# Optimization experiments

Hardware: AMD Instinct MI355X
Metric: run time of the kernel (lower is better)

The kernel has to match this reference:

```python
import jax, jax.numpy as jnp
import numpy as np
from jax import lax

GAMMA_MIN = 1e-4
BIG = 1e9  # finite stand-in for +inf so softmin grads stay nan-free


def _cosine_cost(a, b):
    # F.normalize(dim=-1) with eps=1e-12, then 1 - a_n @ b_n.T
    an = a / jnp.maximum(jnp.linalg.norm(a, axis=-1, keepdims=True), 1e-12)
    bn = b / jnp.maximum(jnp.linalg.norm(b, axis=-1, keepdims=True), 1e-12)
    return 1.0 - an @ bn.T  # (M, N)


def _shift1(v):
    # v[i-1] with BIG padding at i=0
    return jnp.concatenate([jnp.full((1,), BIG, v.dtype), v[:-1]])


def _softdtw(cost, g):
    # Anti-diagonal wavefront DP. Diagonal d holds R[i, d-i], stored as a
    # length-(M+1) vector indexed by i. R[0,0]=0, borders = BIG (inf).
    M, N = cost.shape
    i_arr = jnp.arange(M + 1)
    r0 = jnp.full(M + 1, BIG, cost.dtype).at[0].set(0.0)  # diagonal d=0
    r1 = jnp.full(M + 1, BIG, cost.dtype)                 # diagonal d=1

    def step(carry, d):
        r_dm2, r_dm1 = carry  # diagonals d-2 and d-1
        j = d - i_arr
        valid = (i_arr >= 1) & (i_arr <= M) & (j >= 1) & (j <= N)
        c = cost[jnp.clip(i_arr - 1, 0, M - 1), jnp.clip(j - 1, 0, N - 1)]
        diag = _shift1(r_dm2)   # R[i-1, j-1]
        above = _shift1(r_dm1)  # R[i-1, j]
        left = r_dm1            # R[i,   j-1]
        v = jnp.stack([diag, above, left])  # (3, M+1)
        smin = -g * jax.nn.logsumexp(-v / g, axis=0)
        r_new = jnp.where(valid, c + smin, BIG)
        return (r_dm1, r_new), None

    ds = jnp.arange(2, M + N + 1)
    (_, r_last), _ = lax.scan(step, (r0, r1), ds)
    return r_last[M]  # R[M, N]


def setup_inputs() -> dict:
    key = jax.random.key(0)
    kx, ky = jax.random.split(key)
    M, N, D = 2048, 2048, 1024
    x = jax.random.normal(kx, (M, D), dtype=jnp.float32)
    y = jax.random.normal(ky, (N, D), dtype=jnp.float32)
    gamma = jnp.array(1.0, dtype=jnp.float32)  # learned nn.Parameter
    return {"x": x, "y": y, "gamma": gamma}


def reference(x, y, gamma):
    g = jnp.maximum(jnp.abs(gamma), GAMMA_MIN)
    sdtw = _softdtw(_cosine_cost(x, y), g)
    # normalize=True: subtract 0.5*(sdtw(x,x) + sdtw(y,y))
    sdtw_xx = _softdtw(_cosine_cost(x, x), g)
    sdtw_yy = _softdtw(_cosine_cost(y, y), g)
    return sdtw - 0.5 * (sdtw_xx + sdtw_yy)
```

## Files before the change

### kernel.cpp

```cpp
#include <hip/hip_runtime.h>
#include <hip/hip_bf16.h>
#include <math.h>

#define MDIM 2048
#define KDIM 1024
#define BIGF 1e9f
#define NSTRIP 32

typedef unsigned short ushort;
typedef unsigned int uint;
typedef __attribute__((ext_vector_type(8))) short short8v;
typedef __attribute__((ext_vector_type(8))) ushort ushort8v;
typedef __attribute__((ext_vector_type(4))) float f32x4;
typedef __attribute__((ext_vector_type(4), aligned(4))) float f4u;

__device__ __forceinline__ ushort f2bf(float f) {
  uint b = __builtin_bit_cast(uint, f);
  b += 0x7FFFu + ((b >> 16) & 1u);
  return (ushort)(b >> 16);
}

__global__ __launch_bounds__(256) void normalize_rows(
    const float* __restrict__ x, const float* __restrict__ y,
    ushort* __restrict__ xb, ushort* __restrict__ yb) {
  int wave = (blockIdx.x * blockDim.x + threadIdx.x) >> 6;
  int lane = threadIdx.x & 63;
  const float* src;
  ushort* dst;
  int row;
  if (wave < MDIM) { src = x; dst = xb; row = wave; }
  else             { src = y; dst = yb; row = wave - MDIM; }
  const float* r = src + (size_t)row * KDIM;
  ushort* w = dst + (size_t)row * KDIM;
  float ss = 0.f;
  for (int c = lane * 4; c < KDIM; c += 64 * 4) {
    float4 v = *(const float4*)&r[c];
    ss += v.x * v.x + v.y * v.y + v.z * v.z + v.w * v.w;
  }
  #pragma unroll
  for (int off = 32; off; off >>= 1) ss += __shfl_xor(ss, off, 64);
  float inv = 1.f / fmaxf(sqrtf(ss), 1e-12f);
  for (int c = lane * 4; c < KDIM; c += 64 * 4) {
    float4 v = *(const float4*)&r[c];
    uint2 o;
    o.x = (uint)f2bf(v.x * inv) | ((uint)f2bf(v.y * inv) << 16);
    o.y = (uint)f2bf(v.z * inv) | ((uint)f2bf(v.w * inv) << 16);
    *(uint2*)&w[c] = o;
  }
}

__global__ __launch_bounds__(256) void gemm_cost_mfma(
    const ushort* __restrict__ xb, const ushort* __restrict__ yb,
    float* __restrict__ cost_base, const float* __restrict__ gamma_p) {
  int z = blockIdx.z;
  const ushort* A = (z == 2) ? yb : xb;
  const ushort* B = (z == 0) ? yb : ((z == 1) ? xb : yb);
  float* C = cost_base + (size_t)z * MDIM * MDIM;
  float g = fmaxf(fabsf(gamma_p[0]), 1e-4f);
  float kexp = 1.44269504089f / g;

  __shared__ ushort As[128 * 64];
  __shared__ ushort Bs[128 * 64];

  int tid = threadIdx.x;
  int w = tid >> 6, l = tid & 63;
  int wr = w >> 1, wc = w & 1;
  int abase = blockIdx.y * 128;
  int bbase = blockIdx.x * 128;

  f32x4 acc[4][4] = {};

  for (int k0 = 0; k0 < KDIM; k0 += 64) {
    ushort8v va[4], vb[4];
    #pragma unroll
    for (int q = 0; q < 4; ++q) {
      int slot = q * 256 + tid;
      int row = slot >> 3, sc = slot & 7;
      va[q] = *(const ushort8v*)&A[(size_t)(abase + row) * KDIM + k0 + sc * 8];
      vb[q] = *(const ushort8v*)&B[(size_t)(bbase + row) * KDIM + k0 + sc * 8];
    }
    __syncthreads();
    #pragma unroll
    for (int q = 0; q < 4; ++q) {
      int slot = q * 256 + tid;
      int row = slot >> 3, sc = slot & 7;
      int off = row * 64 + ((sc ^ (row & 7)) << 3);
      *(ushort8v*)&As[off] = va[q];
      *(ushort8v*)&Bs[off] = vb[q];
    }
    __syncthreads();
    #pragma unroll
    for (int kk = 0; kk < 2; ++kk) {
      short8v af[4], bf[4];
      #pragma unroll
      for (int m = 0; m < 4; ++m) {
        int row = wr * 64 + m * 16 + (l & 15);
        int kg = kk * 4 + (l >> 4);
        af[m] = *(const short8v*)&As[row * 64 + ((kg ^ (row & 7)) << 3)];
      }
      #pragma unroll
      for (int n = 0; n < 4; ++n) {
        int row = wc * 64 + n * 16 + (l & 15);
        int kg = kk * 4 + (l >> 4);
        bf[n] = *(const short8v*)&Bs[row * 64 + ((kg ^ (row & 7)) << 3)];
      }
      #pragma unroll
      for (int m = 0; m < 4; ++m)
        #pragma unroll
        for (int n = 0; n < 4; ++n)
          acc[m][n] = __builtin_amdgcn_mfma_f32_16x16x32_bf16(
              af[m], bf[n], acc[m][n], 0, 0, 0);
    }
  }
  #pragma unroll
  for (int m = 0; m < 4; ++m) {
    int row0 = abase + wr * 64 + m * 16 + (l >> 4) * 4;
    #pragma unroll
    for (int n = 0; n < 4; ++n) {
      int col = bbase + wc * 64 + n * 16 + (l & 15);
      f32x4 v = acc[m][n];
      #pragma unroll
      for (int r = 0; r < 4; ++r)
        C[(size_t)(row0 + r) * MDIM + col] = (1.0f - v[r]) * kexp;
    }
  }
}

__device__ __forceinline__ float fexp2(float x) { return __builtin_amdgcn_exp2f(x); }
__device__ __forceinline__ float flog2(float x) { return __builtin_amdgcn_logf(x); }

__device__ __forceinline__ float shr1(float v) {
  int r = __builtin_amdgcn_update_dpp(__builtin_bit_cast(int, v),
                                      __builtin_bit_cast(int, v),
                                      0x138 , 0xF, 0xF, false);
  return __builtin_bit_cast(float, r);
}

__device__ __forceinline__ float aload(const float* p) {
  return __hip_atomic_load(p, __ATOMIC_RELAXED, __HIP_MEMORY_SCOPE_AGENT);
}

__device__ __forceinline__ void stage(f4u (&buf)[16],
                                      const float* __restrict__ crow, int base) {
  #pragma unroll
  for (int k = 0; k < 16; ++k)
    buf[k] = *(const f4u*)&crow[base + 4 * k];
}

__device__ __forceinline__ void stage_edge(f4u (&buf)[16],
                                           const float* __restrict__ crow,
                                           int base) {
  #pragma unroll
  for (int k = 0; k < 16; ++k)
    #pragma unroll
    for (int j = 0; j < 4; ++j) {
      int col = min(max(base + 4 * k + j, 0), MDIM - 1);
      buf[k][j] = crow[col];
    }
}

template <bool FIRST, bool EDGE>
__device__ __forceinline__ void phase_body(
    float& o, float& d, float bqv, const f4u (&cur)[16],
    int cb, int lane, float* __restrict__ bw) {
  const bool l0 = (lane == 0);
  const bool l63 = (lane == 63);
  float h0, h1, h2, h3;
  #pragma unroll
  for (int u = 0; u < 64; ++u) {
    float t = shr1(o);
    float av;
    if (FIRST) {
      av = l0 ? BIGF : t;
    } else {
      float rv = __builtin_bit_cast(
          float, __builtin_amdgcn_readlane(__builtin_bit_cast(int, bqv), u));
      av = l0 ? rv : t;
    }
    float mn, md, mx;
    asm("v_min3_f32 %0, %1, %2, %3" : "=v"(mn) : "v"(d), "v"(av), "v"(o));
    asm("v_med3_f32 %0, %1, %2, %3" : "=v"(md) : "v"(d), "v"(av), "v"(o));
    asm("v_max3_f32 %0, %1, %2, %3" : "=v"(mx) : "v"(d), "v"(av), "v"(o));
    float e = 1.0f + fexp2(mn - md) + fexp2(mn - mx);
    float n = cur[u >> 2][u & 3] + (mn - flog2(e));
    if (EDGE) {
      int c = cb + u - lane;
      bool valid = ((unsigned)c < (unsigned)MDIM);
      n = valid ? n : BIGF;
      if (l63 && valid) bw[c] = n;
    } else {
      if ((u & 3) == 0) h0 = n;
      else if ((u & 3) == 1) h1 = n;
      else if ((u & 3) == 2) h2 = n;
      else {
        h3 = n;
        if (l63) *(f4u*)&bw[cb + u - 66] = (f4u){h0, h1, h2, h3};
      }
    }
    d = av;
    o = n;
  }
}

__global__ __launch_bounds__(64, 1) void softdtw_dp(
    const float* __restrict__ cost_base, float* __restrict__ bottom,
    int* __restrict__ flags) {
  const int bid = blockIdx.x;
  const int z = bid & 7;
  if (z >= 3) return;
  const int s = bid >> 3;
  const int lane = threadIdx.x;

  const float* cost = cost_base + (size_t)z * MDIM * MDIM;
  const float* crow = cost + (size_t)(s * 64 + lane) * MDIM;
  float* bot_z = bottom + (size_t)z * NSTRIP * MDIM;
  const float* bp = bot_z + (size_t)(s > 0 ? s - 1 : 0) * MDIM;
  float* bw = bot_z + (size_t)s * MDIM;
  int* predf = &flags[z * NSTRIP + (s > 0 ? s - 1 : 0)];
  int* myf = &flags[z * NSTRIP + s];

  const int pS0 = 2 * s;
  const int pS1 = 2 * s + 32;

  f4u bufA[16], bufB[16];
  stage_edge(bufA, crow, -lane);

  float o = BIGF;
  float d = (s == 0 && lane == 0) ? 0.0f : BIGF;

  if (lane == 63 && s > 0)
    __hip_atomic_store(myf, pS0, __ATOMIC_RELEASE, __HIP_MEMORY_SCOPE_AGENT);

  int pcache = 0;
  for (int p = pS0; p <= pS1; ++p) {
    const int dq = p - pS0;
    const int cb = dq << 6;
    if (s > 0 && pcache < p) {
      int it = 0;
      do {
        pcache = __hip_atomic_load(predf, __ATOMIC_ACQUIRE,
                                   __HIP_MEMORY_SCOPE_AGENT);
        if (pcache < p) __builtin_amdgcn_s_sleep(1);
      } while (pcache < p && ++it < (1 << 22));
    }
    float bqv = 0.0f;
    if (s > 0) bqv = aload(&bp[min(cb + lane, MDIM - 1)]);
    if (dq < 31) {
      if ((dq & 1) == 0) stage(bufB, crow, cb + 64 - lane);
      else               stage(bufA, crow, cb + 64 - lane);
    } else if (dq == 31) {
      stage_edge(bufA, crow, cb + 64 - lane);
    }
    const bool edge = (dq == 0) || (dq == 32);
    if (s == 0) {
      if ((dq & 1) == 0) {
        if (edge) phase_body<true, true>(o, d, bqv, bufA, cb, lane, bw);
        else      phase_body<true, false>(o, d, bqv, bufA, cb, lane, bw);
      } else {
        phase_body<true, false>(o, d, bqv, bufB, cb, lane, bw);
      }
    } else {
      if ((dq & 1) == 0) {
        if (edge) phase_body<false, true>(o, d, bqv, bufA, cb, lane, bw);
        else      phase_body<false, false>(o, d, bqv, bufA, cb, lane, bw);
      } else {
        phase_body<false, false>(o, d, bqv, bufB, cb, lane, bw);
      }
    }
    if (lane == 63)
      __hip_atomic_store(myf, p + 1, __ATOMIC_RELEASE,
                         __HIP_MEMORY_SCOPE_AGENT);
  }
  if (lane == 63)
    __hip_atomic_store(myf, 1 << 20, __ATOMIC_RELEASE,
                       __HIP_MEMORY_SCOPE_AGENT);
}

__global__ void dtw_init(int* __restrict__ flags) {
  if (threadIdx.x < 3 * NSTRIP) flags[threadIdx.x] = 0;
}

__global__ void combine(const float* __restrict__ bottom,
                        const float* __restrict__ gamma_p,
                        float* __restrict__ out) {
  float g = fmaxf(fabsf(gamma_p[0]), 1e-4f);
  float glog = 0.69314718056f * g;
  float b0 = bottom[0 * NSTRIP * MDIM + (NSTRIP - 1) * MDIM + 2047];
  float b1 = bottom[1 * NSTRIP * MDIM + (NSTRIP - 1) * MDIM + 2047];
  float b2 = bottom[2 * NSTRIP * MDIM + (NSTRIP - 1) * MDIM + 2047];
  out[0] = (b0 - 0.5f * (b1 + b2)) * glog;
}

extern "C" void kernel_launch(void* const* d_in, const int* in_sizes, int n_in,
                              void* d_out, int out_size, void* d_ws, size_t ws_size,
                              hipStream_t stream) {
  const float* x = (const float*)d_in[0];
  const float* y = (const float*)d_in[1];
  const float* gamma = (const float*)d_in[2];
  float* out = (float*)d_out;

  char* ws = (char*)d_ws;
  ushort* xb = (ushort*)ws;
  ushort* yb = (ushort*)(ws + (size_t)4 * 1024 * 1024);
  float* cost = (float*)(ws + (size_t)8 * 1024 * 1024);
  float* bottom = (float*)(ws + (size_t)56 * 1024 * 1024);
  int* flags = (int*)(ws + (size_t)59 * 1024 * 1024);

  normalize_rows<<<(2 * MDIM) / 4, 256, 0, stream>>>(x, y, xb, yb);

  dim3 ggrid(MDIM / 128, MDIM / 128, 3);
  gemm_cost_mfma<<<ggrid, 256, 0, stream>>>(xb, yb, cost, gamma);

  dtw_init<<<1, 128, 0, stream>>>(flags);

  softdtw_dp<<<256, 64, 0, stream>>>(cost, bottom, flags);

  combine<<<1, 1, 0, stream>>>(bottom, gamma, out);
}
```

Baseline: 887.0 us.

## Halve DP phase granularity to 32 columns to shorten inter-strip pipeline latency

Each strip now advances in phases of 32 anti-diagonal steps instead of 64, with 66 phases per strip, and signals the next strip after each one. Successor strips can start sooner, which shortens the fill and drain of the 32-strip wavefront pipeline. The next cost tile and the boundary value are prefetched one phase ahead, with a sched_barrier and a register pin to keep the loads overlapped with compute. The cost is twice as many flag polls and atomic stores, and smaller prefetch batches.

```diff
diff --git a/kernel.cpp b/kernel.cpp
--- a/kernel.cpp
+++ b/kernel.cpp
@@ -140,18 +140,24 @@
   return __hip_atomic_load(p, __ATOMIC_RELAXED, __HIP_MEMORY_SCOPE_AGENT);
 }
 
-__device__ __forceinline__ void stage(f4u (&buf)[16],
-                                      const float* __restrict__ crow, int base) {
-  #pragma unroll
-  for (int k = 0; k < 16; ++k)
+__device__ __forceinline__ void pin8(f4u (&b)[8]) {
+  asm volatile("" : "+v"(b[0]), "+v"(b[1]), "+v"(b[2]), "+v"(b[3]),
+                    "+v"(b[4]), "+v"(b[5]), "+v"(b[6]), "+v"(b[7]));
+}
+
+__device__ __forceinline__ void stage8(f4u (&buf)[8],
+                                       const float* __restrict__ crow,
+                                       int base) {
+  #pragma unroll
+  for (int k = 0; k < 8; ++k)
     buf[k] = *(const f4u*)&crow[base + 4 * k];
 }
 
-__device__ __forceinline__ void stage_edge(f4u (&buf)[16],
-                                           const float* __restrict__ crow,
-                                           int base) {
-  #pragma unroll
-  for (int k = 0; k < 16; ++k)
+__device__ __forceinline__ void stage8_edge(f4u (&buf)[8],
+                                            const float* __restrict__ crow,
+                                            int base) {
+  #pragma unroll
+  for (int k = 0; k < 8; ++k)
     #pragma unroll
     for (int j = 0; j < 4; ++j) {
       int col = min(max(base + 4 * k + j, 0), MDIM - 1);
@@ -160,21 +166,21 @@
 }
 
 template <bool FIRST, bool EDGE>
-__device__ __forceinline__ void phase_body(
-    float& o, float& d, float bqv, const f4u (&cur)[16],
+__device__ __forceinline__ void phase32(
+    float& o, float& d, float bq, const f4u (&cur)[8],
     int cb, int lane, float* __restrict__ bw) {
   const bool l0 = (lane == 0);
   const bool l63 = (lane == 63);
   float h0, h1, h2, h3;
   #pragma unroll
-  for (int u = 0; u < 64; ++u) {
+  for (int u = 0; u < 32; ++u) {
     float t = shr1(o);
     float av;
     if (FIRST) {
       av = l0 ? BIGF : t;
     } else {
       float rv = __builtin_bit_cast(
-          float, __builtin_amdgcn_readlane(__builtin_bit_cast(int, bqv), u));
+          float, __builtin_amdgcn_readlane(__builtin_bit_cast(int, bq), u));
       av = l0 ? rv : t;
     }
     float mn, md, mx;
@@ -202,6 +208,61 @@
   }
 }
 
+template <bool FIRST>
+__device__ __forceinline__ void do_phase(
+    int dq, int s, int lane, f4u (&cur)[8], f4u (&nxt)[8],
+    float& o, float& d, float& bqN,
+    const float* __restrict__ crow, const float* __restrict__ bp,
+    float* __restrict__ bw, int* myf, int* predf, int& pcache) {
+  const int p = 4 * s + dq;
+  const int cb = dq << 5;
+  if (!FIRST && pcache < p) {
+    int it = 0;
+    do {
+      pcache = __hip_atomic_load(predf, __ATOMIC_ACQUIRE,
+                                 __HIP_MEMORY_SCOPE_AGENT);
+      if (pcache < p) __builtin_amdgcn_s_sleep(1);
+    } while (pcache < p && ++it < (1 << 22));
+  }
+  float bq = bqN;
+  if (dq >= 1 && dq <= 62)      stage8(nxt, crow, cb + 32 - lane);
+  else if (dq != 65)            stage8_edge(nxt, crow, cb + 32 - lane);
+  if (!FIRST && dq < 65)
+    bqN = aload(&bp[min(cb + 32 + lane, MDIM - 1)]);
+  __builtin_amdgcn_sched_barrier(0);
+  pin8(cur);
+  const bool edge = (dq < 2) || (dq > 63);
+  if (edge) phase32<FIRST, true>(o, d, bq, cur, cb, lane, bw);
+  else      phase32<FIRST, false>(o, d, bq, cur, cb, lane, bw);
+  if (lane == 63)
+    __hip_atomic_store(myf, p + 1, __ATOMIC_RELEASE,
+                       __HIP_MEMORY_SCOPE_AGENT);
+}
+
+template <bool FIRST>
+__device__ __forceinline__ void run_strip(
+    int s, int lane, const float* __restrict__ crow,
+    const float* __restrict__ bp, float* __restrict__ bw,
+    int* myf, int* predf) {
+  f4u bufA[8], bufB[8];
+  stage8_edge(bufA, crow, -lane);
+  float o = BIGF;
+  float d = (FIRST && lane == 0) ? 0.0f : BIGF;
+  float bqN = 0.0f;
+  if (!FIRST) bqN = aload(&bp[lane]);
+  int pcache = 0;
+  #pragma unroll 1
+  for (int dq2 = 0; dq2 < 66; dq2 += 2) {
+    do_phase<FIRST>(dq2, s, lane, bufA, bufB, o, d, bqN, crow, bp, bw,
+                    myf, predf, pcache);
+    do_phase<FIRST>(dq2 + 1, s, lane, bufB, bufA, o, d, bqN, crow, bp, bw,
+                    myf, predf, pcache);
+  }
+  if (lane == 63)
+    __hip_atomic_store(myf, 1 << 20, __ATOMIC_RELEASE,
+                       __HIP_MEMORY_SCOPE_AGENT);
+}
+
 __global__ __launch_bounds__(64, 1) void softdtw_dp(
     const float* __restrict__ cost_base, float* __restrict__ bottom,
     int* __restrict__ flags) {
@@ -219,61 +280,8 @@
   int* predf = &flags[z * NSTRIP + (s > 0 ? s - 1 : 0)];
   int* myf = &flags[z * NSTRIP + s];
 
-  const int pS0 = 2 * s;
-  const int pS1 = 2 * s + 32;
-
-  f4u bufA[16], bufB[16];
-  stage_edge(bufA, crow, -lane);
-
-  float o = BIGF;
-  float d = (s == 0 && lane == 0) ? 0.0f : BIGF;
-
-  if (lane == 63 && s > 0)
-    __hip_atomic_store(myf, pS0, __ATOMIC_RELEASE, __HIP_MEMORY_SCOPE_AGENT);
-
-  int pcache = 0;
-  for (int p = pS0; p <= pS1; ++p) {
-    const int dq = p - pS0;
-    const int cb = dq << 6;
-    if (s > 0 && pcache < p) {
-      int it = 0;
-      do {
-        pcache = __hip_atomic_load(predf, __ATOMIC_ACQUIRE,
-                                   __HIP_MEMORY_SCOPE_AGENT);
-        if (pcache < p) __builtin_amdgcn_s_sleep(1);
-      } while (pcache < p && ++it < (1 << 22));
-    }
-    float bqv = 0.0f;
-    if (s > 0) bqv = aload(&bp[min(cb + lane, MDIM - 1)]);
-    if (dq < 31) {
-      if ((dq & 1) == 0) stage(bufB, crow, cb + 64 - lane);
-      else               stage(bufA, crow, cb + 64 - lane);
-    } else if (dq == 31) {
-      stage_edge(bufA, crow, cb + 64 - lane);
-    }
-    const bool edge = (dq == 0) || (dq == 32);
-    if (s == 0) {
-      if ((dq & 1) == 0) {
-        if (edge) phase_body<true, true>(o, d, bqv, bufA, cb, lane, bw);
-        else      phase_body<true, false>(o, d, bqv, bufA, cb, lane, bw);
-      } else {
-        phase_body<true, false>(o, d, bqv, bufB, cb, lane, bw);
-      }
-    } else {
-      if ((dq & 1) == 0) {
-        if (edge) phase_body<false, true>(o, d, bqv, bufA, cb, lane, bw);
-        else      phase_body<false, false>(o, d, bqv, bufA, cb, lane, bw);
-      } else {
-        phase_body<false, false>(o, d, bqv, bufB, cb, lane, bw);
-      }
-    }
-    if (lane == 63)
-      __hip_atomic_store(myf, p + 1, __ATOMIC_RELEASE,
-                         __HIP_MEMORY_SCOPE_AGENT);
-  }
-  if (lane == 63)
-    __hip_atomic_store(myf, 1 << 20, __ATOMIC_RELEASE,
-                       __HIP_MEMORY_SCOPE_AGENT);
+  if (s == 0) run_strip<true>(s, lane, crow, bp, bw, myf, predf);
+  else        run_strip<false>(s, lane, crow, bp, bw, myf, predf);
 }
 
 __global__ void dtw_init(int* __restrict__ flags) {
```

New measurement: 1.134 ms. +27.9%, slower.
